# Kernel tuning notes

Measured on AMD Instinct MI355X. Metric: run time of the kernel, lower is better.

Reference implementation:

```python
import jax, jax.numpy as jnp
import numpy as np

# Surrogate spike: forward heaviside, backward 1/(1+5|x|)^2
@jax.custom_vjp
def spike_fn(x):
    return (x >= 0).astype(x.dtype)

def _spike_fwd(x):
    return (x >= 0).astype(x.dtype), x

def _spike_bwd(x, g):
    return (g / (1.0 + 5.0 * jnp.abs(x)) ** 2,)

spike_fn.defvjp(_spike_fwd, _spike_bwd)

B, T, C, H, TDA, NCLS = 512, 1000, 64, 128, 150, 4
EPS = 1e-5


def setup_inputs() -> dict:
    key = jax.random.key(0)
    ks = jax.random.split(key, 16)
    inp = {}
    inp['kin_spikes_seq'] = jax.random.uniform(ks[0], (B, T, C), dtype=jnp.float32)
    inp['tda_features'] = jax.random.normal(ks[1], (B, TDA), dtype=jnp.float32)
    # spike_fc: init normal(mean=0.02, std=0.1), zero bias
    inp['W_fc'] = 0.02 + 0.1 * jax.random.normal(ks[2], (H, C), dtype=jnp.float32)
    inp['b_fc'] = jnp.zeros((H,), jnp.float32)
    # tda_net
    inp['W_t1'] = 0.08 * jax.random.normal(ks[3], (64, TDA), dtype=jnp.float32)
    inp['b_t1'] = jnp.zeros((64,), jnp.float32)
    inp['W_t2'] = 0.12 * jax.random.normal(ks[4], (64, 64), dtype=jnp.float32)
    inp['b_t2'] = jnp.zeros((64,), jnp.float32)
    # classifier: Linear(H+64 -> 128), BN(128), Linear(128 -> NCLS)
    inp['W_c1'] = 0.07 * jax.random.normal(ks[5], (128, H + 64), dtype=jnp.float32)
    inp['b_c1'] = jnp.zeros((128,), jnp.float32)
    inp['bn_gamma'] = jnp.ones((128,), jnp.float32)
    inp['bn_beta'] = jnp.zeros((128,), jnp.float32)
    inp['W_c2'] = 0.09 * jax.random.normal(ks[6], (NCLS, 128), dtype=jnp.float32)
    inp['b_c2'] = jnp.zeros((NCLS,), jnp.float32)
    return inp


def reference(kin_spikes_seq, tda_features, W_fc, b_fc, W_t1, b_t1, W_t2, b_t2,
              W_c1, b_c1, bn_gamma, bn_beta, W_c2, b_c2):
    Bsz, Tlen, _ = kin_spikes_seq.shape
    Hd = W_fc.shape[0]
    # Precompute all per-step input currents with one big GEMM (same math as
    # per-step Linear, since weights are time-invariant).
    currents = jnp.einsum('btc,hc->bth', kin_spikes_seq, W_fc) + b_fc  # [B,T,H]
    cur_t_first = jnp.transpose(currents, (1, 0, 2))  # [T,B,H]

    def step(carry, cur):
        mem, counts = carry
        mem = 0.9 * mem + cur
        spk = spike_fn(mem - 1.0)
        mem = mem * (1.0 - spk)
        return (mem, counts + spk), None

    init = (jnp.zeros((Bsz, Hd), kin_spikes_seq.dtype),
            jnp.zeros((Bsz, Hd), kin_spikes_seq.dtype))
    (mem, spike_counts), _ = jax.lax.scan(step, init, cur_t_first)

    firing_rate = spike_counts / Tlen
    tda_h = jax.nn.relu(tda_features @ W_t1.T + b_t1)
    tda_out = jax.nn.relu(tda_h @ W_t2.T + b_t2)
    fused = jnp.concatenate([firing_rate, tda_out], axis=1)  # [B, H+64]

    h = fused @ W_c1.T + b_c1
    # BatchNorm1d (training-mode batch statistics, biased variance)
    mean = jnp.mean(h, axis=0)
    var = jnp.var(h, axis=0)
    h = (h - mean) * jax.lax.rsqrt(var + EPS) * bn_gamma + bn_beta
    h = jax.nn.relu(h)  # dropout is identity in eval
    out = h @ W_c2.T + b_c2
    return out, spike_counts
```

## Files before the change

kernel.cpp:

```cpp
#include <hip/hip_runtime.h>
#include <stdint.h>

#define BB 512
#define TT 1000
#define CC 64
#define HH 128
#define TDA_F 150
#define NCLS 4
#define EPSV 1e-5f
#define NSEG 8
#define SEGLEN 125
#define WARM 51
#define CPAD 20

typedef _Float16 half8 __attribute__((ext_vector_type(8)));
typedef float floatx4 __attribute__((ext_vector_type(4)));

__device__ __forceinline__ half8 cvt8(const float4& a, const float4& b) {
  half8 r;
  r[0] = (_Float16)a.x; r[1] = (_Float16)a.y;
  r[2] = (_Float16)a.z; r[3] = (_Float16)a.w;
  r[4] = (_Float16)b.x; r[5] = (_Float16)b.y;
  r[6] = (_Float16)b.z; r[7] = (_Float16)b.w;
  return r;
}

__global__ __launch_bounds__(64, 2) void snn_scan(
    const float* __restrict__ kin, const float* __restrict__ Wfc,
    const float* __restrict__ bfc, float* __restrict__ part)
{
  const int lane = threadIdx.x;
  const int q = lane >> 4;
  const int ml = lane & 15;
  const int b = blockIdx.x >> 3;
  const int seg = blockIdx.x & 7;

  const int t0 = (seg == 0) ? 0 : SEGLEN * seg - WARM;
  const int ntiles = (seg == 0) ? 8 : 11;
  const int lo = SEGLEN * seg;
  const int hi = lo + SEGLEN;

  half8 bh[8][2], bl[8][2];
  float bv[8];
#pragma unroll
  for (int ht = 0; ht < 8; ++ht) {
    bv[ht] = bfc[ht * 16 + ml];
#pragma unroll
    for (int kh = 0; kh < 2; ++kh) {
      const float* wp = Wfc + (ht * 16 + ml) * CC + kh * 32 + q * 8;
      float4 w0 = *(const float4*)(wp);
      float4 w1 = *(const float4*)(wp + 4);
      float wv[8] = {w0.x, w0.y, w0.z, w0.w, w1.x, w1.y, w1.z, w1.w};
      half8 h, l;
#pragma unroll
      for (int i = 0; i < 8; ++i) {
        _Float16 x = (_Float16)wv[i];
        h[i] = x;
        l[i] = (_Float16)(wv[i] - (float)x);
      }
      bh[ht][kh] = h;
      bl[ht][kh] = l;
    }
  }

  __shared__ float cur[HH * CPAD];

  const float* ab = kin + ((size_t)b * TT + (t0 + ml)) * CC + q * 8;

  float4 p[2][4];
#pragma unroll
  for (int i = 0; i < 2; ++i) {
    const float* s = ab + i * 16 * CC;
    p[i][0] = *(const float4*)(s);
    p[i][1] = *(const float4*)(s + 4);
    p[i][2] = *(const float4*)(s + 32);
    p[i][3] = *(const float4*)(s + 36);
  }

  float mem0 = 0.f, mem1 = 0.f, cnt0 = 0.f, cnt1 = 0.f;

  for (int c = 0; c < ntiles; ++c) {
    half8 a0 = cvt8(p[c & 1][0], p[c & 1][1]);
    half8 a1 = cvt8(p[c & 1][2], p[c & 1][3]);

    if (c + 2 < ntiles) {
      const float* s = ab + (size_t)(c + 2) * 16 * CC;
      p[c & 1][0] = *(const float4*)(s);
      p[c & 1][1] = *(const float4*)(s + 4);
      p[c & 1][2] = *(const float4*)(s + 32);
      p[c & 1][3] = *(const float4*)(s + 36);
    }

    floatx4 acc[8];
#pragma unroll
    for (int ht = 0; ht < 8; ++ht) {
      floatx4 a = {bv[ht], bv[ht], bv[ht], bv[ht]};
      a = __builtin_amdgcn_mfma_f32_16x16x32_f16(a0, bl[ht][0], a, 0, 0, 0);
      a = __builtin_amdgcn_mfma_f32_16x16x32_f16(a0, bh[ht][0], a, 0, 0, 0);
      a = __builtin_amdgcn_mfma_f32_16x16x32_f16(a1, bl[ht][1], a, 0, 0, 0);
      a = __builtin_amdgcn_mfma_f32_16x16x32_f16(a1, bh[ht][1], a, 0, 0, 0);
      acc[ht] = a;
    }

    if (c >= 1) {
      const float4* r0 = (const float4*)(cur + lane * CPAD);
      const float4* r1 = (const float4*)(cur + (lane + 64) * CPAD);
      float4 v0[4] = {r0[0], r0[1], r0[2], r0[3]};
      float4 v1[4] = {r1[0], r1[1], r1[2], r1[3]};
      const float* f0 = (const float*)v0;
      const float* f1 = (const float*)v1;
      const int tb = t0 + (c - 1) * 16;
#pragma unroll
      for (int s = 0; s < 16; ++s) {
        const int t = tb + s;
        const bool act = (t >= lo) && (t < hi);
        mem0 = fmaf(0.9f, mem0, f0[s]);
        mem1 = fmaf(0.9f, mem1, f1[s]);
        const bool s0 = (mem0 >= 1.0f);
        const bool s1 = (mem1 >= 1.0f);
        cnt0 += (act && s0) ? 1.0f : 0.0f;
        cnt1 += (act && s1) ? 1.0f : 0.0f;
        mem0 = s0 ? 0.0f : mem0;
        mem1 = s1 ? 0.0f : mem1;
      }
    }

#pragma unroll
    for (int ht = 0; ht < 8; ++ht) {
      float4 st = {acc[ht][0], acc[ht][1], acc[ht][2], acc[ht][3]};
      *(float4*)(cur + (ht * 16 + ml) * CPAD + q * 4) = st;
    }
  }

  {
    const float4* r0 = (const float4*)(cur + lane * CPAD);
    const float4* r1 = (const float4*)(cur + (lane + 64) * CPAD);
    float4 v0[4] = {r0[0], r0[1], r0[2], r0[3]};
    float4 v1[4] = {r1[0], r1[1], r1[2], r1[3]};
    const float* f0 = (const float*)v0;
    const float* f1 = (const float*)v1;
    const int tb = t0 + (ntiles - 1) * 16;
#pragma unroll
    for (int s = 0; s < 16; ++s) {
      const int t = tb + s;
      const bool act = (t >= lo) && (t < hi);
      mem0 = fmaf(0.9f, mem0, f0[s]);
      mem1 = fmaf(0.9f, mem1, f1[s]);
      const bool s0 = (mem0 >= 1.0f);
      const bool s1 = (mem1 >= 1.0f);
      cnt0 += (act && s0) ? 1.0f : 0.0f;
      cnt1 += (act && s1) ? 1.0f : 0.0f;
      mem0 = s0 ? 0.0f : mem0;
      mem1 = s1 ? 0.0f : mem1;
    }
  }

  float* pp = part + ((size_t)(seg * BB + b)) * HH;
  pp[lane] = cnt0;
  pp[lane + 64] = cnt1;
}

__global__ __launch_bounds__(HH) void fused_head(
    const float* __restrict__ part, const float* __restrict__ tda,
    const float* __restrict__ W1, const float* __restrict__ b1,
    const float* __restrict__ W2, const float* __restrict__ b2,
    const float* __restrict__ Wc1, const float* __restrict__ bc1,
    float* __restrict__ counts_out, float* __restrict__ hbuf)
{
  const int b = blockIdx.x, j = threadIdx.x;
  __shared__ float x[TDA_F];
  __shared__ float h1[64];
  __shared__ float f[HH + 64];

  float c = 0.0f;
#pragma unroll
  for (int s = 0; s < NSEG; ++s) c += part[((size_t)(s * BB + b)) * HH + j];
  counts_out[b * HH + j] = c;
  f[j] = c * (1.0f / TT);
  for (int i = j; i < TDA_F; i += HH) x[i] = tda[b * TDA_F + i];
  __syncthreads();
  if (j < 64) {
    float acc = b1[j];
    const float* wr = W1 + j * TDA_F;
#pragma unroll 5
    for (int i = 0; i < TDA_F; ++i) acc = fmaf(x[i], wr[i], acc);
    h1[j] = fmaxf(acc, 0.0f);
  }
  __syncthreads();
  if (j < 64) {
    float acc = b2[j];
    const float* wr = W2 + j * 64;
#pragma unroll
    for (int i = 0; i < 64; ++i) acc = fmaf(h1[i], wr[i], acc);
    f[HH + j] = fmaxf(acc, 0.0f);
  }
  __syncthreads();
  float acc = bc1[j];
  const float* wr = Wc1 + j * (HH + 64);
#pragma unroll 4
  for (int i = 0; i < HH + 64; ++i) acc = fmaf(f[i], wr[i], acc);
  hbuf[b * HH + j] = acc;
}

__global__ __launch_bounds__(HH) void classifier2(
    const float* __restrict__ hbuf,
    const float* __restrict__ gamma, const float* __restrict__ beta,
    const float* __restrict__ Wc2, const float* __restrict__ bc2,
    float* __restrict__ out)
{
  const int b = blockIdx.x, j = threadIdx.x;
  float s0 = 0.f, q0 = 0.f, s1 = 0.f, q1 = 0.f;
  for (int r = 0; r < BB; r += 2) {
    float v0 = hbuf[r * HH + j];
    float v1 = hbuf[(r + 1) * HH + j];
    s0 += v0; q0 = fmaf(v0, v0, q0);
    s1 += v1; q1 = fmaf(v1, v1, q1);
  }
  const float mean = (s0 + s1) * (1.0f / BB);
  const float var = (q0 + q1) * (1.0f / BB) - mean * mean;
  const float rstd = rsqrtf(var + EPSV);

  float hn = (hbuf[b * HH + j] - mean) * rstd * gamma[j] + beta[j];
  hn = fmaxf(hn, 0.0f);

  __shared__ float red[NCLS][HH];
#pragma unroll
  for (int k = 0; k < NCLS; ++k) red[k][j] = hn * Wc2[k * HH + j];
  __syncthreads();
  for (int off = HH / 2; off >= 1; off >>= 1) {
    if (j < off) {
#pragma unroll
      for (int k = 0; k < NCLS; ++k) red[k][j] += red[k][j + off];
    }
    __syncthreads();
  }
  if (j < NCLS) out[b * NCLS + j] = red[j][0] + bc2[j];
}

extern "C" void kernel_launch(void* const* d_in, const int* in_sizes, int n_in,
                              void* d_out, int out_size, void* d_ws, size_t ws_size,
                              hipStream_t stream)
{
  const float* kin  = (const float*)d_in[0];
  const float* tda  = (const float*)d_in[1];
  const float* Wfc  = (const float*)d_in[2];
  const float* bfc  = (const float*)d_in[3];
  const float* Wt1  = (const float*)d_in[4];
  const float* bt1  = (const float*)d_in[5];
  const float* Wt2  = (const float*)d_in[6];
  const float* bt2  = (const float*)d_in[7];
  const float* Wc1  = (const float*)d_in[8];
  const float* bc1  = (const float*)d_in[9];
  const float* gam  = (const float*)d_in[10];
  const float* bet  = (const float*)d_in[11];
  const float* Wc2  = (const float*)d_in[12];
  const float* bc2  = (const float*)d_in[13];

  float* out    = (float*)d_out;
  float* counts = out + BB * NCLS;

  float* part = (float*)d_ws;
  float* hbuf = part + NSEG * BB * HH;

  snn_scan<<<BB * NSEG, 64, 0, stream>>>(kin, Wfc, bfc, part);
  fused_head<<<BB, HH, 0, stream>>>(part, tda, Wt1, bt1, Wt2, bt2,
                                    Wc1, bc1, counts, hbuf);
  classifier2<<<BB, HH, 0, stream>>>(hbuf, gam, bet, Wc2, bc2, out);
}
```

Before: 314.2 us.

## Drop split-fp16 weight correction and simplify scan pipeline in snn_scan

Removes the hi/lo fp16 split of the fc weights, halving the MFMA count per tile, and stores each tile's currents to shared memory right after computing them. The one-tile software pipeline between MFMA output and the serial scan is dropped, and launch bounds are raised to 3 waves per SIMD. Together these cut matrix work and register pressure. In exchange the currents lose weight precision, which can flip threshold crossings and change spike counts, and the MFMA work no longer overlaps the scan.

Result: slower. 325.0 us (+3.4%).

```diff
diff --git a/kernel.cpp b/kernel.cpp
--- a/kernel.cpp
+++ b/kernel.cpp
@@ -25,7 +25,7 @@
   return r;
 }
 
-__global__ __launch_bounds__(64, 2) void snn_scan(
+__global__ __launch_bounds__(64, 3) void snn_scan(
     const float* __restrict__ kin, const float* __restrict__ Wfc,
     const float* __restrict__ bfc, float* __restrict__ part)
 {
@@ -40,7 +40,7 @@
   const int lo = SEGLEN * seg;
   const int hi = lo + SEGLEN;
 
-  half8 bh[8][2], bl[8][2];
+  half8 bfrag[8][2];
   float bv[8];
 #pragma unroll
   for (int ht = 0; ht < 8; ++ht) {
@@ -50,16 +50,7 @@
       const float* wp = Wfc + (ht * 16 + ml) * CC + kh * 32 + q * 8;
       float4 w0 = *(const float4*)(wp);
       float4 w1 = *(const float4*)(wp + 4);
-      float wv[8] = {w0.x, w0.y, w0.z, w0.w, w1.x, w1.y, w1.z, w1.w};
-      half8 h, l;
-#pragma unroll
-      for (int i = 0; i < 8; ++i) {
-        _Float16 x = (_Float16)wv[i];
-        h[i] = x;
-        l[i] = (_Float16)(wv[i] - (float)x);
-      }
-      bh[ht][kh] = h;
-      bl[ht][kh] = l;
+      bfrag[ht][kh] = cvt8(w0, w1);
     }
   }
 
@@ -91,31 +82,30 @@
       p[c & 1][3] = *(const float4*)(s + 36);
     }
 
-    floatx4 acc[8];
 #pragma unroll
     for (int ht = 0; ht < 8; ++ht) {
       floatx4 a = {bv[ht], bv[ht], bv[ht], bv[ht]};
-      a = __builtin_amdgcn_mfma_f32_16x16x32_f16(a0, bl[ht][0], a, 0, 0, 0);
-      a = __builtin_amdgcn_mfma_f32_16x16x32_f16(a0, bh[ht][0], a, 0, 0, 0);
-      a = __builtin_amdgcn_mfma_f32_16x16x32_f16(a1, bl[ht][1], a, 0, 0, 0);
-      a = __builtin_amdgcn_mfma_f32_16x16x32_f16(a1, bh[ht][1], a, 0, 0, 0);
-      acc[ht] = a;
-    }
-
-    if (c >= 1) {
-      const float4* r0 = (const float4*)(cur + lane * CPAD);
-      const float4* r1 = (const float4*)(cur + (lane + 64) * CPAD);
-      float4 v0[4] = {r0[0], r0[1], r0[2], r0[3]};
-      float4 v1[4] = {r1[0], r1[1], r1[2], r1[3]};
-      const float* f0 = (const float*)v0;
-      const float* f1 = (const float*)v1;
-      const int tb = t0 + (c - 1) * 16;
-#pragma unroll
-      for (int s = 0; s < 16; ++s) {
-        const int t = tb + s;
+      a = __builtin_amdgcn_mfma_f32_16x16x32_f16(a0, bfrag[ht][0], a, 0, 0, 0);
+      a = __builtin_amdgcn_mfma_f32_16x16x32_f16(a1, bfrag[ht][1], a, 0, 0, 0);
+      float4 st = {a[0], a[1], a[2], a[3]};
+      *(float4*)(cur + (ht * 16 + ml) * CPAD + q * 4) = st;
+    }
+
+    const float4* r0 = (const float4*)(cur + lane * CPAD);
+    const float4* r1 = (const float4*)(cur + (lane + 64) * CPAD);
+    const int tb = t0 + c * 16;
+#pragma unroll
+    for (int i = 0; i < 4; ++i) {
+      float4 v0 = r0[i];
+      float4 v1 = r1[i];
+#pragma unroll
+      for (int k = 0; k < 4; ++k) {
+        const int t = tb + i * 4 + k;
         const bool act = (t >= lo) && (t < hi);
-        mem0 = fmaf(0.9f, mem0, f0[s]);
-        mem1 = fmaf(0.9f, mem1, f1[s]);
+        const float f0 = (k == 0) ? v0.x : (k == 1) ? v0.y : (k == 2) ? v0.z : v0.w;
+        const float f1 = (k == 0) ? v1.x : (k == 1) ? v1.y : (k == 2) ? v1.z : v1.w;
+        mem0 = fmaf(0.9f, mem0, f0);
+        mem1 = fmaf(0.9f, mem1, f1);
         const bool s0 = (mem0 >= 1.0f);
         const bool s1 = (mem1 >= 1.0f);
         cnt0 += (act && s0) ? 1.0f : 0.0f;
@@ -123,35 +113,6 @@
         mem0 = s0 ? 0.0f : mem0;
         mem1 = s1 ? 0.0f : mem1;
       }
-    }
-
-#pragma unroll
-    for (int ht = 0; ht < 8; ++ht) {
-      float4 st = {acc[ht][0], acc[ht][1], acc[ht][2], acc[ht][3]};
-      *(float4*)(cur + (ht * 16 + ml) * CPAD + q * 4) = st;
-    }
-  }
-
-  {
-    const float4* r0 = (const float4*)(cur + lane * CPAD);
-    const float4* r1 = (const float4*)(cur + (lane + 64) * CPAD);
-    float4 v0[4] = {r0[0], r0[1], r0[2], r0[3]};
-    float4 v1[4] = {r1[0], r1[1], r1[2], r1[3]};
-    const float* f0 = (const float*)v0;
-    const float* f1 = (const float*)v1;
-    const int tb = t0 + (ntiles - 1) * 16;
-#pragma unroll
-    for (int s = 0; s < 16; ++s) {
-      const int t = tb + s;
-      const bool act = (t >= lo) && (t < hi);
-      mem0 = fmaf(0.9f, mem0, f0[s]);
-      mem1 = fmaf(0.9f, mem1, f1[s]);
-      const bool s0 = (mem0 >= 1.0f);
-      const bool s1 = (mem1 >= 1.0f);
-      cnt0 += (act && s0) ? 1.0f : 0.0f;
-      cnt1 += (act && s1) ? 1.0f : 0.0f;
-      mem0 = s0 ? 0.0f : mem0;
-      mem1 = s1 ? 0.0f : mem1;
     }
   }
 
```
